# Performance work log

Hardware: AMD Instinct MI355X
Metric: run time of the kernel (lower is better)

Reference implementation:

```python
import jax, jax.numpy as jnp
import numpy as np

B, N, F = 2, 2048, 512
W = 128          # winlen
D = 512          # d_model


def setup_inputs() -> dict:
    key = jax.random.key(0)
    k1, k2 = jax.random.split(key)
    x = jax.random.normal(k1, (B, N, F), dtype=jnp.float32)
    # Linear(in_features, 3*d_model, bias=False): weight shape (3D, F)
    W_lin = jax.random.normal(k2, (3 * D, F), dtype=jnp.float32) * 0.02
    return {"x": x, "W_lin": W_lin}


def reference(x, W_lin):
    b, n, f = x.shape
    qkv = jnp.einsum("bnf,ef->bne", x, W_lin)           # [B,N,3D]
    q, k, v = jnp.split(qkv, 3, axis=-1)                  # each [B,N,D]
    # Causal sliding window: position n sees [n-W+1, n], zero-padded on left.
    pad = W - 1
    k_pad = jnp.pad(k, ((0, 0), (pad, 0), (0, 0)))        # [B,N+W-1,D]
    v_pad = jnp.pad(v, ((0, 0), (pad, 0), (0, 0)))
    idx = jnp.arange(n)[:, None] + jnp.arange(W)[None, :]  # [N,W] -> k_pad[n+w]
    kr = k_pad[:, idx, :]                                  # [B,N,W,D]
    vr = v_pad[:, idx, :]                                  # [B,N,W,D]
    # NOTE: original forward does NOT apply attn_scale -> no scaling here.
    logits = jnp.einsum("bnd,bnwd->bnw", q, kr)           # [B,N,W]
    attn = jax.nn.softmax(logits, axis=-1)
    out = jnp.einsum("bnw,bnwd->bnd", attn, vr)           # [B,N,D]
    return out
```

## Files before the change

### kernel.cpp

```cpp
#include <hip/hip_runtime.h>
#include <cstdint>
#include <cstddef>

typedef unsigned short u16;
typedef unsigned int u32;
typedef u16 u16x4 __attribute__((ext_vector_type(4)));
typedef u16 u16x8 __attribute__((ext_vector_type(8)));
typedef u32 u32x4 __attribute__((ext_vector_type(4)));
typedef _Float16 f16x8 __attribute__((ext_vector_type(8)));
typedef float f32x4 __attribute__((ext_vector_type(4)));

#define B_   2
#define N_   2048
#define F_   512
#define D_   512
#define W_   128
#define E3   1536
#define MTOT 4096
#define XELEMS (MTOT * F_)
#define WELEMS (E3 * F_)
#define QK_ELEMS (MTOT * D_)

__device__ __forceinline__ u16 f2h(float f) {
  return __builtin_bit_cast(u16, (_Float16)f);
}

__device__ __forceinline__ f32x4 mfma_f16(u16x8 a, u16x8 b, f32x4 c) {
  return __builtin_amdgcn_mfma_f32_16x16x32_f16(
      __builtin_bit_cast(f16x8, a), __builtin_bit_cast(f16x8, b), c, 0, 0, 0);
}

__device__ __forceinline__ void glds16(const u16* g, u16* l) {
  __builtin_amdgcn_global_load_lds(
      (const __attribute__((address_space(1))) void*)g,
      (__attribute__((address_space(3))) void*)l, 16, 0, 0);
}

__global__ __launch_bounds__(256) void cvt_f16(const float* __restrict__ X,
                                               const float* __restrict__ Wl,
                                               u16* __restrict__ Xf, u16* __restrict__ Wf) {
  const int i = blockIdx.x * 256 + threadIdx.x;
  const int n4X = XELEMS / 4;
  u16x4 h;
  if (i < n4X) {
    float4 v = ((const float4*)X)[i];
    h.x = f2h(v.x); h.y = f2h(v.y); h.z = f2h(v.z); h.w = f2h(v.w);
    ((u16x4*)Xf)[i] = h;
  } else {
    int j = i - n4X;
    float4 v = ((const float4*)Wl)[j];
    h.x = f2h(v.x); h.y = f2h(v.y); h.z = f2h(v.z); h.w = f2h(v.w);
    ((u16x4*)Wf)[j] = h;
  }
}

#define TM 128
#define TE 128
#define BK 32

__global__ __launch_bounds__(256) void qkv_gemm(const u16* __restrict__ Xf,
                                                const u16* __restrict__ Wf,
                                                u16* __restrict__ Qf,
                                                u16* __restrict__ Kf,
                                                u16* __restrict__ Vt) {
  __shared__ __align__(16) u16 smem[16896];
  u16* sA = smem;
  u16* sB = smem + 4096;

  const int tid = threadIdx.x;
  const int m0 = blockIdx.x * TM;
  const int e0 = blockIdx.y * TE;
  const int lane = tid & 63;
  const int wave = tid >> 6;
  const int wm = (wave >> 1) * 64;
  const int we = (wave & 1) * 64;
  const int qd = lane >> 4;
  const int l16 = lane & 15;

  const int lrow = lane >> 2;
  const int cg = (lane & 3) ^ ((lrow >> 1) & 3);
  const int lkc = cg * 8;

  f32x4 acc[4][4];
#pragma unroll
  for (int i = 0; i < 4; ++i)
#pragma unroll
    for (int j = 0; j < 4; ++j) acc[i][j] = (f32x4){0.f, 0.f, 0.f, 0.f};

  const int r0 = wave * 32;
  const size_t ga0 = (size_t)(m0 + r0 + lrow) * F_ + lkc;
  const size_t ga1 = (size_t)(m0 + r0 + 16 + lrow) * F_ + lkc;
  const size_t gb0 = (size_t)(e0 + r0 + lrow) * F_ + lkc;
  const size_t gb1 = (size_t)(e0 + r0 + 16 + lrow) * F_ + lkc;
  u16* lA0 = sA + r0 * 32;
  u16* lA1 = sA + (r0 + 16) * 32;
  u16* lB0 = sB + r0 * 32;
  u16* lB1 = sB + (r0 + 16) * 32;

  const int swz = (l16 >> 1) & 3;
  const int rdoff = (qd ^ swz) * 8;

  for (int k0 = 0; k0 < F_; k0 += BK) {
    glds16(Xf + ga0 + k0, lA0);
    glds16(Xf + ga1 + k0, lA1);
    glds16(Wf + gb0 + k0, lB0);
    glds16(Wf + gb1 + k0, lB1);
    __syncthreads();

    u16x8 fA[4], fB[4];
#pragma unroll
    for (int mi = 0; mi < 4; ++mi)
      fA[mi] = *(const u16x8*)&sA[(wm + mi * 16 + l16) * 32 + rdoff];
#pragma unroll
    for (int ei = 0; ei < 4; ++ei)
      fB[ei] = *(const u16x8*)&sB[(we + ei * 16 + l16) * 32 + rdoff];
#pragma unroll
    for (int mi = 0; mi < 4; ++mi)
#pragma unroll
      for (int ei = 0; ei < 4; ++ei)
        acc[mi][ei] = mfma_f16(fA[mi], fB[ei], acc[mi][ei]);
    __syncthreads();
  }

  const int third = e0 >> 9;
  if (third < 2) {
    u16* P = third ? Kf : Qf;
    const int ecol0 = (e0 & 511) + we;
#pragma unroll
    for (int mi = 0; mi < 4; ++mi)
#pragma unroll
      for (int ei = 0; ei < 4; ++ei)
#pragma unroll
        for (int r = 0; r < 4; ++r) {
          int row = m0 + wm + mi * 16 + qd * 4 + r;
          int col = ecol0 + ei * 16 + l16;
          P[(size_t)row * D_ + col] = f2h(acc[mi][ei][r]);
        }
  } else {
    u16* vbuf = smem + wave * 4224;
#pragma unroll
    for (int mi = 0; mi < 4; ++mi)
#pragma unroll
      for (int ei = 0; ei < 4; ++ei)
#pragma unroll
        for (int r2 = 0; r2 < 2; ++r2) {
          int e_in = ei * 16 + l16;
          int m_in = mi * 16 + qd * 4 + r2 * 2;
          u32 p = (u32)f2h(acc[mi][ei][r2 * 2]) |
                  ((u32)f2h(acc[mi][ei][r2 * 2 + 1]) << 16);
          *(u32*)&vbuf[e_in * 66 + m_in] = p;
        }
    __builtin_amdgcn_s_waitcnt(0);
    const int dbase = (e0 - 1024) + we;
    const int mb = (m0 & 2047) + wm;
    const int bb = m0 >> 11;
    u16* vt = Vt + (size_t)bb * (D_ * N_);
#pragma unroll
    for (int it = 0; it < 4; ++it) {
      int e_in = it * 16 + (lane >> 2);
      int mc = lane & 3;
      u32 q0[8];
#pragma unroll
      for (int c4 = 0; c4 < 8; ++c4)
        q0[c4] = *(const u32*)&vbuf[e_in * 66 + mc * 16 + c4 * 2];
      u16* gp = vt + (size_t)(dbase + e_in) * N_ + mb + mc * 16;
      *(u32x4*)gp = (u32x4){q0[0], q0[1], q0[2], q0[3]};
      *(u32x4*)(gp + 8) = (u32x4){q0[4], q0[5], q0[6], q0[7]};
    }
  }
}

#define TQA 16
#define SA 200
#define SP 208

__global__ __launch_bounds__(512) void attn_kernel(const u16* __restrict__ Qf,
                                                   const u16* __restrict__ Kf,
                                                   const u16* __restrict__ Vt,
                                                   float* __restrict__ Out) {
  const int m0 = blockIdx.x * TQA;
  const int b = m0 >> 11;
  const int n0 = m0 & 2047;
  const int t = threadIdx.x;
  const int lane = t & 63;
  const int w = t >> 6;
  const int qd = lane >> 4;
  const int l16 = lane & 15;

  __shared__ __align__(16) float att[2][TQA][SA];
  __shared__ __align__(16) u16 pS[TQA][SP];

  const int jw = w & 3;
  const int kh = w >> 2;

  f32x4 acc[3];
#pragma unroll
  for (int nt = 0; nt < 3; ++nt) acc[nt] = (f32x4){0.f, 0.f, 0.f, 0.f};

  const size_t qrow = (size_t)(m0 + l16) * D_ + qd * 8;
  for (int ks = kh * 8; ks < kh * 8 + 8; ++ks) {
    u16x8 qv = *(const u16x8*)(Qf + qrow + ks * 32);
#pragma unroll
    for (int nt = 0; nt < 3; ++nt) {
      int j = (jw * 3 + nt) * 16 + l16;
      int rl = n0 - 128 + j;
      int rg = b * N_ + (rl > 0 ? rl : 0);
      u16x8 kv = *(const u16x8*)(Kf + (size_t)rg * D_ + ks * 32 + qd * 8);
      acc[nt] = mfma_f16(qv, kv, acc[nt]);
    }
  }
#pragma unroll
  for (int nt = 0; nt < 3; ++nt)
#pragma unroll
    for (int r = 0; r < 4; ++r)
      att[kh][qd * 4 + r][(jw * 3 + nt) * 16 + l16] = acc[nt][r];
  __syncthreads();

  {
    const int i = t >> 5;
    const int c = t & 31;
    float ev[6];
    float mx = -1e30f;
#pragma unroll
    for (int s = 0; s < 6; ++s) {
      int j = c * 6 + s;
      bool inw = (j >= i + 1) && (j <= i + 128);
      float v = -1e30f;
      if (inw) v = (n0 - 128 + j < 0) ? 0.f : att[0][i][j] + att[1][i][j];
      ev[s] = v;
      mx = fmaxf(mx, v);
    }
    mx = fmaxf(mx, __shfl_xor(mx, 1));
    mx = fmaxf(mx, __shfl_xor(mx, 2));
    mx = fmaxf(mx, __shfl_xor(mx, 4));
    mx = fmaxf(mx, __shfl_xor(mx, 8));
    mx = fmaxf(mx, __shfl_xor(mx, 16));
    float sum = 0.f;
#pragma unroll
    for (int s = 0; s < 6; ++s) {
      ev[s] = (ev[s] > -1e29f) ? __expf(ev[s] - mx) : 0.f;
      sum += ev[s];
    }
    sum += __shfl_xor(sum, 1);
    sum += __shfl_xor(sum, 2);
    sum += __shfl_xor(sum, 4);
    sum += __shfl_xor(sum, 8);
    sum += __shfl_xor(sum, 16);
    const float inv = 1.f / sum;
#pragma unroll
    for (int s = 0; s < 6; ++s) {
      int j = c * 6 + s;
      bool zv = (n0 - 128 + j) < 0;
      pS[i][j] = zv ? (u16)0 : f2h(ev[s] * inv);
    }
  }
  __syncthreads();

  f32x4 oacc[4];
#pragma unroll
  for (int nt = 0; nt < 4; ++nt) oacc[nt] = (f32x4){0.f, 0.f, 0.f, 0.f};

  const u16* vtb = Vt + (size_t)b * (D_ * N_);
  for (int kk = 0; kk < 6; ++kk) {
    u16x8 pa = *(const u16x8*)&pS[l16][kk * 32 + qd * 8];
    const int rl = n0 - 128 + kk * 32 + qd * 8;
#pragma unroll
    for (int nt = 0; nt < 4; ++nt) {
      int d = w * 64 + nt * 16 + l16;
      u16x8 vv = *(const u16x8*)(vtb + (size_t)d * N_ + rl);
      oacc[nt] = mfma_f16(pa, vv, oacc[nt]);
    }
  }
#pragma unroll
  for (int nt = 0; nt < 4; ++nt)
#pragma unroll
    for (int r = 0; r < 4; ++r)
      Out[(size_t)(m0 + qd * 4 + r) * D_ + w * 64 + nt * 16 + l16] = oacc[nt][r];
}

extern "C" void kernel_launch(void* const* d_in, const int* in_sizes, int n_in,
                              void* d_out, int out_size, void* d_ws, size_t ws_size,
                              hipStream_t stream) {
  const float* x = (const float*)d_in[0];
  const float* wl = (const float*)d_in[1];
  float* out = (float*)d_out;

  u16* Xf = (u16*)d_ws;
  u16* Wf = Xf + XELEMS;
  u16* Qf = Wf + WELEMS;
  u16* Kf = Qf + QK_ELEMS;
  u16* Vt = Kf + QK_ELEMS;

  cvt_f16<<<(XELEMS + WELEMS) / 4 / 256, 256, 0, stream>>>(x, wl, Xf, Wf);
  dim3 g1(MTOT / TM, E3 / TE);
  qkv_gemm<<<g1, 256, 0, stream>>>(Xf, Wf, Qf, Kf, Vt);
  attn_kernel<<<MTOT / TQA, 512, 0, stream>>>(Qf, Kf, Vt, out);
}
```

Before: 96.56 us.

## Fuse convert, QKV GEMM and attention into one cooperative persistent kernel

After: 177.1 us. +83.5%, slower.

```diff
diff --git a/kernel.cpp b/kernel.cpp
--- a/kernel.cpp
+++ b/kernel.cpp
@@ -1,12 +1,16 @@
 #include <hip/hip_runtime.h>
+#include <hip/hip_cooperative_groups.h>
 #include <cstdint>
 #include <cstddef>
+
+namespace cg = cooperative_groups;
 
 typedef unsigned short u16;
 typedef unsigned int u32;
 typedef u16 u16x4 __attribute__((ext_vector_type(4)));
 typedef u16 u16x8 __attribute__((ext_vector_type(8)));
 typedef u32 u32x4 __attribute__((ext_vector_type(4)));
+typedef _Float16 f16x2 __attribute__((ext_vector_type(2)));
 typedef _Float16 f16x8 __attribute__((ext_vector_type(8)));
 typedef float f32x4 __attribute__((ext_vector_type(4)));
 
@@ -21,261 +25,273 @@
 #define WELEMS (E3 * F_)
 #define QK_ELEMS (MTOT * D_)
 
+#define TQA 16
+#define SA 200
+#define SP 208
+
 __device__ __forceinline__ u16 f2h(float f) {
   return __builtin_bit_cast(u16, (_Float16)f);
 }
-
+__device__ __forceinline__ u32 pk2h(float a, float b) {
+  return __builtin_bit_cast(u32, __builtin_amdgcn_cvt_pkrtz(a, b));
+}
 __device__ __forceinline__ f32x4 mfma_f16(u16x8 a, u16x8 b, f32x4 c) {
   return __builtin_amdgcn_mfma_f32_16x16x32_f16(
       __builtin_bit_cast(f16x8, a), __builtin_bit_cast(f16x8, b), c, 0, 0, 0);
 }
-
 __device__ __forceinline__ void glds16(const u16* g, u16* l) {
   __builtin_amdgcn_global_load_lds(
       (const __attribute__((address_space(1))) void*)g,
       (__attribute__((address_space(3))) void*)l, 16, 0, 0);
 }
 
-__global__ __launch_bounds__(256) void cvt_f16(const float* __restrict__ X,
+__global__ __launch_bounds__(512, 2) void mega(const float* __restrict__ X,
                                                const float* __restrict__ Wl,
-                                               u16* __restrict__ Xf, u16* __restrict__ Wf) {
-  const int i = blockIdx.x * 256 + threadIdx.x;
-  const int n4X = XELEMS / 4;
-  u16x4 h;
-  if (i < n4X) {
-    float4 v = ((const float4*)X)[i];
-    h.x = f2h(v.x); h.y = f2h(v.y); h.z = f2h(v.z); h.w = f2h(v.w);
-    ((u16x4*)Xf)[i] = h;
-  } else {
-    int j = i - n4X;
-    float4 v = ((const float4*)Wl)[j];
-    h.x = f2h(v.x); h.y = f2h(v.y); h.z = f2h(v.z); h.w = f2h(v.w);
-    ((u16x4*)Wf)[j] = h;
-  }
-}
-
-#define TM 128
-#define TE 128
-#define BK 32
-
-__global__ __launch_bounds__(256) void qkv_gemm(const u16* __restrict__ Xf,
-                                                const u16* __restrict__ Wf,
-                                                u16* __restrict__ Qf,
-                                                u16* __restrict__ Kf,
-                                                u16* __restrict__ Vt) {
-  __shared__ __align__(16) u16 smem[16896];
-  u16* sA = smem;
-  u16* sB = smem + 4096;
-
-  const int tid = threadIdx.x;
-  const int m0 = blockIdx.x * TM;
-  const int e0 = blockIdx.y * TE;
-  const int lane = tid & 63;
-  const int wave = tid >> 6;
-  const int wm = (wave >> 1) * 64;
-  const int we = (wave & 1) * 64;
+                                               u16* __restrict__ Xf, u16* __restrict__ Wf,
+                                               u16* __restrict__ Qf, u16* __restrict__ Kf,
+                                               u16* __restrict__ Vt,
+                                               float* __restrict__ Out) {
+  __shared__ __align__(16) u32 shraw[8320];
+  u16* sm16 = (u16*)shraw;
+
+  cg::grid_group grid = cg::this_grid();
+
+  const int t = threadIdx.x;
+  const int lane = t & 63;
+  const int wave = t >> 6;
   const int qd = lane >> 4;
   const int l16 = lane & 15;
 
-  const int lrow = lane >> 2;
-  const int cg = (lane & 3) ^ ((lrow >> 1) & 3);
-  const int lkc = cg * 8;
-
-  f32x4 acc[4][4];
-#pragma unroll
-  for (int i = 0; i < 4; ++i)
-#pragma unroll
-    for (int j = 0; j < 4; ++j) acc[i][j] = (f32x4){0.f, 0.f, 0.f, 0.f};
-
-  const int r0 = wave * 32;
-  const size_t ga0 = (size_t)(m0 + r0 + lrow) * F_ + lkc;
-  const size_t ga1 = (size_t)(m0 + r0 + 16 + lrow) * F_ + lkc;
-  const size_t gb0 = (size_t)(e0 + r0 + lrow) * F_ + lkc;
-  const size_t gb1 = (size_t)(e0 + r0 + 16 + lrow) * F_ + lkc;
-  u16* lA0 = sA + r0 * 32;
-  u16* lA1 = sA + (r0 + 16) * 32;
-  u16* lB0 = sB + r0 * 32;
-  u16* lB1 = sB + (r0 + 16) * 32;
-
-  const int swz = (l16 >> 1) & 3;
-  const int rdoff = (qd ^ swz) * 8;
-
-  for (int k0 = 0; k0 < F_; k0 += BK) {
-    glds16(Xf + ga0 + k0, lA0);
-    glds16(Xf + ga1 + k0, lA1);
-    glds16(Wf + gb0 + k0, lB0);
-    glds16(Wf + gb1 + k0, lB1);
+  {
+    const int n4X = XELEMS / 4;
+    const int n4T = (XELEMS + WELEMS) / 4;
+    for (int i = blockIdx.x * 512 + t; i < n4T; i += 256 * 512) {
+      u16x4 h;
+      if (i < n4X) {
+        float4 v = ((const float4*)X)[i];
+        h.x = f2h(v.x); h.y = f2h(v.y); h.z = f2h(v.z); h.w = f2h(v.w);
+        ((u16x4*)Xf)[i] = h;
+      } else {
+        int j = i - n4X;
+        float4 v = ((const float4*)Wl)[j];
+        h.x = f2h(v.x); h.y = f2h(v.y); h.z = f2h(v.z); h.w = f2h(v.w);
+        ((u16x4*)Wf)[j] = h;
+      }
+    }
+  }
+  grid.sync();
+
+  if (blockIdx.x < 192) {
+    u16* sA = sm16;
+    u16* sB = sm16 + 8192;
+
+    const int my = blockIdx.x / 12;
+    const int ey = blockIdx.x % 12;
+    const int m0 = my * 256;
+    const int e0 = ey * 128;
+    const int wm = (wave >> 1) * 64;
+    const int we = (wave & 1) * 64;
+
+    const int lrow = lane >> 2;
+    const int cg_ = (lane & 3) ^ ((lrow >> 1) & 3);
+    const int lkc = cg_ * 8;
+
+    f32x4 acc[4][4];
+#pragma unroll
+    for (int i = 0; i < 4; ++i)
+#pragma unroll
+      for (int j = 0; j < 4; ++j) acc[i][j] = (f32x4){0.f, 0.f, 0.f, 0.f};
+
+    const u16* gsrc[3];
+    u16* ldst[3];
+#pragma unroll
+    for (int s = 0; s < 3; ++s) {
+      int ib = wave * 3 + s;
+      if (ib < 16) {
+        int row0 = ib * 16;
+        gsrc[s] = Xf + (size_t)(m0 + row0 + lrow) * F_ + lkc;
+        ldst[s] = sA + row0 * 32;
+      } else {
+        int row0 = (ib - 16) * 16;
+        gsrc[s] = Wf + (size_t)(e0 + row0 + lrow) * F_ + lkc;
+        ldst[s] = sB + row0 * 32;
+      }
+    }
+
+    const int swz = (l16 >> 1) & 3;
+    const int rdoff = (qd ^ swz) * 8;
+
+    for (int k0 = 0; k0 < F_; k0 += 32) {
+#pragma unroll
+      for (int s = 0; s < 3; ++s) glds16(gsrc[s] + k0, ldst[s]);
+      __syncthreads();
+
+      u16x8 fA[4], fB[4];
+#pragma unroll
+      for (int mi = 0; mi < 4; ++mi)
+        fA[mi] = *(const u16x8*)&sA[(wm + mi * 16 + l16) * 32 + rdoff];
+#pragma unroll
+      for (int ei = 0; ei < 4; ++ei)
+        fB[ei] = *(const u16x8*)&sB[(we + ei * 16 + l16) * 32 + rdoff];
+#pragma unroll
+      for (int mi = 0; mi < 4; ++mi)
+#pragma unroll
+        for (int ei = 0; ei < 4; ++ei)
+          acc[mi][ei] = mfma_f16(fA[mi], fB[ei], acc[mi][ei]);
+      __syncthreads();
+    }
+
+    const int third = e0 >> 9;
+    if (third < 2) {
+      u16* P = third ? Kf : Qf;
+      const int ecol0 = (e0 & 511) + we;
+      const int odd = l16 & 1;
+#pragma unroll
+      for (int mi = 0; mi < 4; ++mi)
+#pragma unroll
+        for (int ei = 0; ei < 4; ++ei) {
+          float x0 = acc[mi][ei][0], x1 = acc[mi][ei][1];
+          float x2 = acc[mi][ei][2], x3 = acc[mi][ei][3];
+          float t0 = __shfl_xor(x0, 1), t1 = __shfl_xor(x1, 1);
+          float t2 = __shfl_xor(x2, 1), t3 = __shfl_xor(x3, 1);
+          u32 pa = odd ? pk2h(t2, x2) : pk2h(x0, t0);
+          u32 pb = odd ? pk2h(t3, x3) : pk2h(x1, t1);
+          int mrow = m0 + wm + mi * 16 + qd * 4 + odd * 2;
+          int colp = ecol0 + ei * 16 + (l16 & ~1);
+          *(u32*)(P + (size_t)mrow * D_ + colp) = pa;
+          *(u32*)(P + (size_t)(mrow + 1) * D_ + colp) = pb;
+        }
+    } else {
+      u16* vbuf = sm16 + wave * 1056;
+      const int dbase = (e0 - 1024) + we;
+      const int mb = (m0 & 2047) + wm;
+      const int bb = m0 >> 11;
+      u16* vt = Vt + (size_t)bb * (D_ * N_);
+#pragma unroll
+      for (int ei = 0; ei < 4; ++ei) {
+#pragma unroll
+        for (int mi = 0; mi < 4; ++mi)
+#pragma unroll
+          for (int r2 = 0; r2 < 2; ++r2) {
+            int m_in = mi * 16 + qd * 4 + r2 * 2;
+            u32 p = pk2h(acc[mi][ei][r2 * 2], acc[mi][ei][r2 * 2 + 1]);
+            *(u32*)&vbuf[l16 * 66 + m_in] = p;
+          }
+        __builtin_amdgcn_s_waitcnt(0);
+        int er = lane >> 2;
+        int mc = lane & 3;
+        u32 q0[8];
+#pragma unroll
+        for (int c4 = 0; c4 < 8; ++c4)
+          q0[c4] = *(const u32*)&vbuf[er * 66 + mc * 16 + c4 * 2];
+        u16* gp = vt + (size_t)(dbase + ei * 16 + er) * N_ + mb + mc * 16;
+        *(u32x4*)gp = (u32x4){q0[0], q0[1], q0[2], q0[3]};
+        *(u32x4*)(gp + 8) = (u32x4){q0[4], q0[5], q0[6], q0[7]};
+        __builtin_amdgcn_s_waitcnt(0);
+      }
+    }
+  }
+  grid.sync();
+
+  {
+    float* attp = (float*)shraw;
+    u16* pSp = sm16 + 12800;
+
+    const int m0 = blockIdx.x * TQA;
+    const int b = m0 >> 11;
+    const int n0 = m0 & 2047;
+    const int jw = wave & 3;
+    const int kh = wave >> 2;
+
+    f32x4 acc[3];
+#pragma unroll
+    for (int nt = 0; nt < 3; ++nt) acc[nt] = (f32x4){0.f, 0.f, 0.f, 0.f};
+
+    const size_t qrow = (size_t)(m0 + l16) * D_ + qd * 8;
+    for (int ks = kh * 8; ks < kh * 8 + 8; ++ks) {
+      u16x8 qv = *(const u16x8*)(Qf + qrow + ks * 32);
+#pragma unroll
+      for (int nt = 0; nt < 3; ++nt) {
+        int j = (jw * 3 + nt) * 16 + l16;
+        int rl = n0 - 128 + j;
+        int rg = b * N_ + (rl > 0 ? rl : 0);
+        u16x8 kv = *(const u16x8*)(Kf + (size_t)rg * D_ + ks * 32 + qd * 8);
+        acc[nt] = mfma_f16(qv, kv, acc[nt]);
+      }
+    }
+#pragma unroll
+    for (int nt = 0; nt < 3; ++nt)
+#pragma unroll
+      for (int r = 0; r < 4; ++r)
+        attp[kh * (TQA * SA) + (qd * 4 + r) * SA + (jw * 3 + nt) * 16 + l16] =
+            acc[nt][r];
     __syncthreads();
 
-    u16x8 fA[4], fB[4];
-#pragma unroll
-    for (int mi = 0; mi < 4; ++mi)
-      fA[mi] = *(const u16x8*)&sA[(wm + mi * 16 + l16) * 32 + rdoff];
-#pragma unroll
-    for (int ei = 0; ei < 4; ++ei)
-      fB[ei] = *(const u16x8*)&sB[(we + ei * 16 + l16) * 32 + rdoff];
-#pragma unroll
-    for (int mi = 0; mi < 4; ++mi)
-#pragma unroll
-      for (int ei = 0; ei < 4; ++ei)
-        acc[mi][ei] = mfma_f16(fA[mi], fB[ei], acc[mi][ei]);
+    {
+      const int i = t >> 5;
+      const int c = t & 31;
+      float ev[6];
+      float mx = -1e30f;
+#pragma unroll
+      for (int s = 0; s < 6; ++s) {
+        int j = c * 6 + s;
+        bool inw = (j >= i + 1) && (j <= i + 128);
+        float v = -1e30f;
+        if (inw)
+          v = (n0 - 128 + j < 0)
+                  ? 0.f
+                  : attp[i * SA + j] + attp[TQA * SA + i * SA + j];
+        ev[s] = v;
+        mx = fmaxf(mx, v);
+      }
+      mx = fmaxf(mx, __shfl_xor(mx, 1));
+      mx = fmaxf(mx, __shfl_xor(mx, 2));
+      mx = fmaxf(mx, __shfl_xor(mx, 4));
+      mx = fmaxf(mx, __shfl_xor(mx, 8));
+      mx = fmaxf(mx, __shfl_xor(mx, 16));
+      float sum = 0.f;
+#pragma unroll
+      for (int s = 0; s < 6; ++s) {
+        ev[s] = (ev[s] > -1e29f) ? __expf(ev[s] - mx) : 0.f;
+        sum += ev[s];
+      }
+      sum += __shfl_xor(sum, 1);
+      sum += __shfl_xor(sum, 2);
+      sum += __shfl_xor(sum, 4);
+      sum += __shfl_xor(sum, 8);
+      sum += __shfl_xor(sum, 16);
+      const float inv = 1.f / sum;
+#pragma unroll
+      for (int s = 0; s < 6; ++s) {
+        int j = c * 6 + s;
+        bool zv = (n0 - 128 + j) < 0;
+        pSp[i * SP + j] = zv ? (u16)0 : f2h(ev[s] * inv);
+      }
+    }
     __syncthreads();
+
+    f32x4 oacc[4];
+#pragma unroll
+    for (int nt = 0; nt < 4; ++nt) oacc[nt] = (f32x4){0.f, 0.f, 0.f, 0.f};
+
+    const u16* vtb = Vt + (size_t)b * (D_ * N_);
+    for (int kk = 0; kk < 6; ++kk) {
+      u16x8 pa = *(const u16x8*)&pSp[l16 * SP + kk * 32 + qd * 8];
+      const int rl = n0 - 128 + kk * 32 + qd * 8;
+#pragma unroll
+      for (int nt = 0; nt < 4; ++nt) {
+        int d = wave * 64 + nt * 16 + l16;
+        u16x8 vv = *(const u16x8*)(vtb + (size_t)d * N_ + rl);
+        oacc[nt] = mfma_f16(pa, vv, oacc[nt]);
+      }
+    }
+#pragma unroll
+    for (int nt = 0; nt < 4; ++nt)
+#pragma unroll
+      for (int r = 0; r < 4; ++r)
+        Out[(size_t)(m0 + qd * 4 + r) * D_ + wave * 64 + nt * 16 + l16] =
+            oacc[nt][r];
   }
-
-  const int third = e0 >> 9;
-  if (third < 2) {
-    u16* P = third ? Kf : Qf;
-    const int ecol0 = (e0 & 511) + we;
-#pragma unroll
-    for (int mi = 0; mi < 4; ++mi)
-#pragma unroll
-      for (int ei = 0; ei < 4; ++ei)
-#pragma unroll
-        for (int r = 0; r < 4; ++r) {
-          int row = m0 + wm + mi * 16 + qd * 4 + r;
-          int col = ecol0 + ei * 16 + l16;
-          P[(size_t)row * D_ + col] = f2h(acc[mi][ei][r]);
-        }
-  } else {
-    u16* vbuf = smem + wave * 4224;
-#pragma unroll
-    for (int mi = 0; mi < 4; ++mi)
-#pragma unroll
-      for (int ei = 0; ei < 4; ++ei)
-#pragma unroll
-        for (int r2 = 0; r2 < 2; ++r2) {
-          int e_in = ei * 16 + l16;
-          int m_in = mi * 16 + qd * 4 + r2 * 2;
-          u32 p = (u32)f2h(acc[mi][ei][r2 * 2]) |
-                  ((u32)f2h(acc[mi][ei][r2 * 2 + 1]) << 16);
-          *(u32*)&vbuf[e_in * 66 + m_in] = p;
-        }
-    __builtin_amdgcn_s_waitcnt(0);
-    const int dbase = (e0 - 1024) + we;
-    const int mb = (m0 & 2047) + wm;
-    const int bb = m0 >> 11;
-    u16* vt = Vt + (size_t)bb * (D_ * N_);
-#pragma unroll
-    for (int it = 0; it < 4; ++it) {
-      int e_in = it * 16 + (lane >> 2);
-      int mc = lane & 3;
-      u32 q0[8];
-#pragma unroll
-      for (int c4 = 0; c4 < 8; ++c4)
-        q0[c4] = *(const u32*)&vbuf[e_in * 66 + mc * 16 + c4 * 2];
-      u16* gp = vt + (size_t)(dbase + e_in) * N_ + mb + mc * 16;
-      *(u32x4*)gp = (u32x4){q0[0], q0[1], q0[2], q0[3]};
-      *(u32x4*)(gp + 8) = (u32x4){q0[4], q0[5], q0[6], q0[7]};
-    }
-  }
-}
-
-#define TQA 16
-#define SA 200
-#define SP 208
-
-__global__ __launch_bounds__(512) void attn_kernel(const u16* __restrict__ Qf,
-                                                   const u16* __restrict__ Kf,
-                                                   const u16* __restrict__ Vt,
-                                                   float* __restrict__ Out) {
-  const int m0 = blockIdx.x * TQA;
-  const int b = m0 >> 11;
-  const int n0 = m0 & 2047;
-  const int t = threadIdx.x;
-  const int lane = t & 63;
-  const int w = t >> 6;
-  const int qd = lane >> 4;
-  const int l16 = lane & 15;
-
-  __shared__ __align__(16) float att[2][TQA][SA];
-  __shared__ __align__(16) u16 pS[TQA][SP];
-
-  const int jw = w & 3;
-  const int kh = w >> 2;
-
-  f32x4 acc[3];
-#pragma unroll
-  for (int nt = 0; nt < 3; ++nt) acc[nt] = (f32x4){0.f, 0.f, 0.f, 0.f};
-
-  const size_t qrow = (size_t)(m0 + l16) * D_ + qd * 8;
-  for (int ks = kh * 8; ks < kh * 8 + 8; ++ks) {
-    u16x8 qv = *(const u16x8*)(Qf + qrow + ks * 32);
-#pragma unroll
-    for (int nt = 0; nt < 3; ++nt) {
-      int j = (jw * 3 + nt) * 16 + l16;
-      int rl = n0 - 128 + j;
-      int rg = b * N_ + (rl > 0 ? rl : 0);
-      u16x8 kv = *(const u16x8*)(Kf + (size_t)rg * D_ + ks * 32 + qd * 8);
-      acc[nt] = mfma_f16(qv, kv, acc[nt]);
-    }
-  }
-#pragma unroll
-  for (int nt = 0; nt < 3; ++nt)
-#pragma unroll
-    for (int r = 0; r < 4; ++r)
-      att[kh][qd * 4 + r][(jw * 3 + nt) * 16 + l16] = acc[nt][r];
-  __syncthreads();
-
-  {
-    const int i = t >> 5;
-    const int c = t & 31;
-    float ev[6];
-    float mx = -1e30f;
-#pragma unroll
-    for (int s = 0; s < 6; ++s) {
-      int j = c * 6 + s;
-      bool inw = (j >= i + 1) && (j <= i + 128);
-      float v = -1e30f;
-      if (inw) v = (n0 - 128 + j < 0) ? 0.f : att[0][i][j] + att[1][i][j];
-      ev[s] = v;
-      mx = fmaxf(mx, v);
-    }
-    mx = fmaxf(mx, __shfl_xor(mx, 1));
-    mx = fmaxf(mx, __shfl_xor(mx, 2));
-    mx = fmaxf(mx, __shfl_xor(mx, 4));
-    mx = fmaxf(mx, __shfl_xor(mx, 8));
-    mx = fmaxf(mx, __shfl_xor(mx, 16));
-    float sum = 0.f;
-#pragma unroll
-    for (int s = 0; s < 6; ++s) {
-      ev[s] = (ev[s] > -1e29f) ? __expf(ev[s] - mx) : 0.f;
-      sum += ev[s];
-    }
-    sum += __shfl_xor(sum, 1);
-    sum += __shfl_xor(sum, 2);
-    sum += __shfl_xor(sum, 4);
-    sum += __shfl_xor(sum, 8);
-    sum += __shfl_xor(sum, 16);
-    const float inv = 1.f / sum;
-#pragma unroll
-    for (int s = 0; s < 6; ++s) {
-      int j = c * 6 + s;
-      bool zv = (n0 - 128 + j) < 0;
-      pS[i][j] = zv ? (u16)0 : f2h(ev[s] * inv);
-    }
-  }
-  __syncthreads();
-
-  f32x4 oacc[4];
-#pragma unroll
-  for (int nt = 0; nt < 4; ++nt) oacc[nt] = (f32x4){0.f, 0.f, 0.f, 0.f};
-
-  const u16* vtb = Vt + (size_t)b * (D_ * N_);
-  for (int kk = 0; kk < 6; ++kk) {
-    u16x8 pa = *(const u16x8*)&pS[l16][kk * 32 + qd * 8];
-    const int rl = n0 - 128 + kk * 32 + qd * 8;
-#pragma unroll
-    for (int nt = 0; nt < 4; ++nt) {
-      int d = w * 64 + nt * 16 + l16;
-      u16x8 vv = *(const u16x8*)(vtb + (size_t)d * N_ + rl);
-      oacc[nt] = mfma_f16(pa, vv, oacc[nt]);
-    }
-  }
-#pragma unroll
-  for (int nt = 0; nt < 4; ++nt)
-#pragma unroll
-    for (int r = 0; r < 4; ++r)
-      Out[(size_t)(m0 + qd * 4 + r) * D_ + w * 64 + nt * 16 + l16] = oacc[nt][r];
 }
 
 extern "C" void kernel_launch(void* const* d_in, const int* in_sizes, int n_in,
@@ -291,8 +307,7 @@
   u16* Kf = Qf + QK_ELEMS;
   u16* Vt = Kf + QK_ELEMS;
 
-  cvt_f16<<<(XELEMS + WELEMS) / 4 / 256, 256, 0, stream>>>(x, wl, Xf, Wf);
-  dim3 g1(MTOT / TM, E3 / TE);
-  qkv_gemm<<<g1, 256, 0, stream>>>(Xf, Wf, Qf, Kf, Vt);
-  attn_kernel<<<MTOT / TQA, 512, 0, stream>>>(Qf, Kf, Vt, out);
-}
+  void* kargs[] = {(void*)&x, (void*)&wl, (void*)&Xf, (void*)&Wf,
+                   (void*)&Qf, (void*)&Kf, (void*)&Vt, (void*)&out};
+  hipLaunchCooperativeKernel((void*)mega, dim3(256), dim3(512), kargs, 0, stream);
+}
```
